# Kernel optimization log

Measured on AMD Instinct MI355X. Metric: run time of the kernel, lower is better.

## Reference

```python
import jax, jax.numpy as jnp
import numpy as np

EPS = 1e-5
NUM_HEADS = 12
PATCH = 16

def layernorm(x, g, b):
    m = jnp.mean(x, axis=-1, keepdims=True)
    v = jnp.var(x, axis=-1, keepdims=True)
    return (x - m) / jnp.sqrt(v + EPS) * g + b

def setup_inputs() -> dict:
    key = jax.random.key(0)
    ks = jax.random.split(key, 10)
    B, C, H, D, L = 32, 3, 224, 768, 12
    Dff, NCLS = 3072, 5
    N = (H // PATCH) ** 2 + 1  # 197 tokens incl. cls
    def rn(k, shape, s=0.02):
        return jax.random.normal(k, shape, jnp.float32) * s
    return {
        "x": jax.random.normal(ks[0], (B, C, H, H), jnp.float32),
        "conv_w": rn(ks[1], (D, C, PATCH, PATCH)),
        "conv_b": jnp.zeros((D,), jnp.float32),
        "cls_token": rn(ks[2], (1, 1, D)),
        "pos_embed": rn(ks[3], (1, N, D)),
        "ln1_g": jnp.ones((L, D), jnp.float32), "ln1_b": jnp.zeros((L, D), jnp.float32),
        "qkv_w": rn(ks[4], (L, D, 3 * D)), "qkv_b": jnp.zeros((L, 3 * D), jnp.float32),
        "proj_w": rn(ks[5], (L, D, D)), "proj_b": jnp.zeros((L, D), jnp.float32),
        "ln2_g": jnp.ones((L, D), jnp.float32), "ln2_b": jnp.zeros((L, D), jnp.float32),
        "fc1_w": rn(ks[6], (L, D, Dff)), "fc1_b": jnp.zeros((L, Dff), jnp.float32),
        "fc2_w": rn(ks[7], (L, Dff, D)), "fc2_b": jnp.zeros((L, D), jnp.float32),
        "norm_g": jnp.ones((D,), jnp.float32), "norm_b": jnp.zeros((D,), jnp.float32),
        "head_w": rn(ks[8], (D, NCLS)), "head_b": jnp.zeros((NCLS,), jnp.float32),
    }

def reference(x, conv_w, conv_b, cls_token, pos_embed,
              ln1_g, ln1_b, qkv_w, qkv_b, proj_w, proj_b,
              ln2_g, ln2_b, fc1_w, fc1_b, fc2_w, fc2_b,
              norm_g, norm_b, head_w, head_b):
    B = x.shape[0]
    D = conv_w.shape[0]
    HD = D // NUM_HEADS
    scale = HD ** -0.5
    # patch embedding: conv stride=kernel=16 -> [B, D, 14, 14]
    p = jax.lax.conv_general_dilated(
        x, conv_w, (PATCH, PATCH), 'VALID',
        dimension_numbers=('NCHW', 'OIHW', 'NCHW')) + conv_b[None, :, None, None]
    tok = p.reshape(B, D, -1).transpose(0, 2, 1)  # [B, Np, D]
    tok = jnp.concatenate([jnp.broadcast_to(cls_token, (B, 1, D)), tok], axis=1)
    tok = tok + pos_embed  # [B, N, D]; dropout is identity at eval

    def block(h, params):
        l1g, l1b, qw, qb, pw, pb, l2g, l2b, f1w, f1b, f2w, f2b = params
        y = layernorm(h, l1g, l1b)
        qkv = (y @ qw + qb).reshape(B, -1, 3, NUM_HEADS, HD)
        q, k, v = qkv[:, :, 0], qkv[:, :, 1], qkv[:, :, 2]  # [B, N, H, HD]
        attn = jax.nn.softmax(jnp.einsum('bqhd,bkhd->bhqk', q, k) * scale, axis=-1)
        o = jnp.einsum('bhqk,bkhd->bqhd', attn, v).reshape(B, -1, D)
        h = h + (o @ pw + pb)
        y = layernorm(h, l2g, l2b)
        h = h + (jax.nn.gelu(y @ f1w + f1b, approximate=False) @ f2w + f2b)
        return h, None

    tok, _ = jax.lax.scan(
        block, tok,
        (ln1_g, ln1_b, qkv_w, qkv_b, proj_w, proj_b,
         ln2_g, ln2_b, fc1_w, fc1_b, fc2_w, fc2_b))
    cls = layernorm(tok, norm_g, norm_b)[:, 0]  # [B, D]
    return cls @ head_w + head_b  # [B, num_classes]
```

## Files before the change

kernel.cpp:

```cpp
#include <hip/hip_runtime.h>
#include <hip/hip_bf16.h>
#include <math.h>

#define B_      32
#define NTOK    197
#define NPATCH  196
#define D_      768
#define DFF     3072
#define L_      12
#define NH      12
#define HD      64
#define NCLS    5
#define MTOK    (B_ * NTOK)
#define MPAD    6400
#define MPATCH  (B_ * NPATCH)
#define KPAD    224
#define KS_STR  72
#define VT_STR  232

typedef __attribute__((ext_vector_type(8))) short short8;
typedef __attribute__((ext_vector_type(4))) float floatx4;

static __device__ inline short f2bf(float f) {
  __hip_bfloat16 h = __float2bfloat16(f);
  short s; __builtin_memcpy(&s, &h, 2); return s;
}

__global__ __launch_bounds__(256) void cls_pos_kernel(
    const float* __restrict__ cls, const float* __restrict__ pos,
    float* __restrict__ tok) {
  int i = blockIdx.x * 256 + threadIdx.x;
  if (i < B_ * D_) {
    int b = i / D_, d = i % D_;
    tok[(size_t)b * NTOK * D_ + d] = cls[d] + pos[d];
  }
}

__global__ __launch_bounds__(256) void cvt_kernel(
    const float* __restrict__ src, short* __restrict__ dst, int n) {
  int i = blockIdx.x * 256 + threadIdx.x;
  if (i < n) dst[i] = f2bf(src[i]);
}

__global__ __launch_bounds__(256) void wconv_all_kernel(
    const float* __restrict__ qw, const float* __restrict__ pw,
    const float* __restrict__ f1w, const float* __restrict__ f2w,
    short* __restrict__ wq, short* __restrict__ wp,
    short* __restrict__ w1, short* __restrict__ w2) {
  int id = blockIdx.x;
  const float* W; short* Wt; int K, N, t;
  if (id < 1728)      { W = qw;  Wt = wq; K = 768;  N = 2304; t = id; }
  else if (id < 2304) { W = pw;  Wt = wp; K = 768;  N = 768;  t = id - 1728; }
  else if (id < 4608) { W = f1w; Wt = w1; K = 768;  N = 3072; t = id - 2304; }
  else                { W = f2w; Wt = w2; K = 3072; N = 768;  t = id - 4608; }
  int ntn = N >> 5;
  int k0 = (t / ntn) * 32, n0 = (t % ntn) * 32;
  __shared__ float tt[32][33];
  int tid = threadIdx.x;
#pragma unroll
  for (int q = 0; q < 4; q++) {
    int e = q * 256 + tid;
    int rk = e >> 5, cn = e & 31;
    tt[rk][cn] = W[(size_t)(k0 + rk) * N + n0 + cn];
  }
  __syncthreads();
#pragma unroll
  for (int q = 0; q < 4; q++) {
    int e = q * 256 + tid;
    int rn = e >> 5, ck = e & 31;
    Wt[(size_t)(n0 + rn) * K + k0 + ck] = f2bf(tt[ck][rn]);
  }
}

__global__ __launch_bounds__(256) void im2col_kernel(
    const float* __restrict__ x, short* __restrict__ Abf) {
  int i = blockIdx.x * 256 + threadIdx.x;
  if (i >= MPATCH * D_) return;
  int row = i / D_, col = i % D_;
  int b = row / NPATCH, n = row % NPATCH;
  int ph = n / 14, pw = n % 14;
  int c = col >> 8, r = col & 255;
  int kh = r >> 4, kw = r & 15;
  Abf[i] = f2bf(x[(((size_t)b * 3 + c) * 224 + (ph * 16 + kh)) * 224 + (pw * 16 + kw)]);
}

__global__ __launch_bounds__(256) void patch_scatter_kernel(
    const float* __restrict__ po, const float* __restrict__ pos,
    float* __restrict__ tok) {
  int i = blockIdx.x * 256 + threadIdx.x;
  if (i >= MPATCH * D_) return;
  int row = i / D_, col = i % D_;
  int b = row / NPATCH, n = row % NPATCH;
  tok[((size_t)b * NTOK + 1 + n) * D_ + col] = po[i] + pos[(size_t)(1 + n) * D_ + col];
}

template <bool OBF>
__global__ __launch_bounds__(256) void ln_kernel(
    const float* __restrict__ in, void* __restrict__ out,
    const float* __restrict__ g, const float* __restrict__ bt,
    long rs_in) {
  int row = blockIdx.x;
  const float* xr = in + (size_t)row * rs_in;
  int tid = threadIdx.x;
  float v0 = xr[tid], v1 = xr[tid + 256], v2 = xr[tid + 512];
  float s = v0 + v1 + v2;
#pragma unroll
  for (int off = 32; off; off >>= 1) s += __shfl_xor(s, off);
  __shared__ float red1[4], red2[4];
  int wid = tid >> 6, lane = tid & 63;
  if (lane == 0) red1[wid] = s;
  __syncthreads();
  float mean = (red1[0] + red1[1] + red1[2] + red1[3]) * (1.f / 768.f);
  float d0 = v0 - mean, d1 = v1 - mean, d2 = v2 - mean;
  float s2 = d0 * d0 + d1 * d1 + d2 * d2;
#pragma unroll
  for (int off = 32; off; off >>= 1) s2 += __shfl_xor(s2, off);
  if (lane == 0) red2[wid] = s2;
  __syncthreads();
  float var = (red2[0] + red2[1] + red2[2] + red2[3]) * (1.f / 768.f);
  float rstd = rsqrtf(var + 1e-5f);
  float o0 = d0 * rstd * g[tid]       + bt[tid];
  float o1 = d1 * rstd * g[tid + 256] + bt[tid + 256];
  float o2 = d2 * rstd * g[tid + 512] + bt[tid + 512];
  if (OBF) {
    short* yr = (short*)out + (size_t)row * D_;
    yr[tid] = f2bf(o0); yr[tid + 256] = f2bf(o1); yr[tid + 512] = f2bf(o2);
  } else {
    float* yr = (float*)out + (size_t)row * D_;
    yr[tid] = o0; yr[tid + 256] = o1; yr[tid + 512] = o2;
  }
}

template <int BM, bool OBF, bool RES, bool GELU_, bool SPLITK = false>
__global__ __launch_bounds__(256) void gemm_db_kernel(
    const short* __restrict__ A, const short* __restrict__ Wt,
    const float* __restrict__ bias, const float* __restrict__ res,
    void* __restrict__ Cout, int M, int N, int K, int kslice) {
  constexpr int NBI = (BM == 128) ? 2 : 4;
  __shared__ short As[2][BM * 32];
  __shared__ short Bs[2][128 * 32];
  const int tid = threadIdx.x;
  const int lane = tid & 63;
  const int wid = tid >> 6;
  const int wave_m = (BM == 128) ? (wid >> 1) : 0;
  const int wave_n = (BM == 128) ? (wid & 1) : wid;
  const int mbase = blockIdx.y * BM;
  const int nbase = blockIdx.x * 128;
  const int kbase = SPLITK ? blockIdx.z * kslice : 0;

  const int lrow = lane >> 2;
  const int kbg = (lane & 3) ^ ((lane >> 3) & 3);

  const short* gA0 = A + (size_t)(mbase + wid * 32 + lrow) * K + kbase + kbg * 8;
  const short* gA1 = gA0 + 16 * (size_t)K;
  const int brow0 = (BM == 128) ? (wid * 32) : (wid * 64);
  const short* gB[NBI];
  gB[0] = Wt + (size_t)(nbase + brow0 + lrow) * K + kbase + kbg * 8;
#pragma unroll
  for (int c = 1; c < NBI; c++) gB[c] = gB[0] + (size_t)c * 16 * K;

  typedef const __attribute__((address_space(1))) unsigned* gp_t;
  typedef __attribute__((address_space(3))) unsigned* lp_t;
  const int aoff = wid * 1024;
  const int boff = brow0 * 32;

  __builtin_amdgcn_global_load_lds((gp_t)(const void*)gA0, (lp_t)(void*)(&As[0][aoff]), 16, 0, 0);
  __builtin_amdgcn_global_load_lds((gp_t)(const void*)gA1, (lp_t)(void*)(&As[0][aoff + 512]), 16, 0, 0);
#pragma unroll
  for (int c = 0; c < NBI; c++)
    __builtin_amdgcn_global_load_lds((gp_t)(const void*)gB[c], (lp_t)(void*)(&Bs[0][boff + c * 512]), 16, 0, 0);

  floatx4 zero = {0.f, 0.f, 0.f, 0.f};
  floatx4 acc[4][4];
#pragma unroll
  for (int i = 0; i < 4; i++)
#pragma unroll
    for (int j = 0; j < 4; j++) acc[i][j] = zero;

  const int quad = lane >> 4;
  const int l15 = lane & 15;
  const int s = quad ^ ((l15 >> 1) & 3);

  const int niter = kslice >> 5;
  for (int it = 0; it < niter; it++) {
    const int cur = it & 1, nxt = cur ^ 1;
    __syncthreads();
    if (it + 1 < niter) {
      const int ks = (it + 1) << 5;
      __builtin_amdgcn_global_load_lds((gp_t)(const void*)(gA0 + ks), (lp_t)(void*)(&As[nxt][aoff]), 16, 0, 0);
      __builtin_amdgcn_global_load_lds((gp_t)(const void*)(gA1 + ks), (lp_t)(void*)(&As[nxt][aoff + 512]), 16, 0, 0);
#pragma unroll
      for (int c = 0; c < NBI; c++)
        __builtin_amdgcn_global_load_lds((gp_t)(const void*)(gB[c] + ks), (lp_t)(void*)(&Bs[nxt][boff + c * 512]), 16, 0, 0);
    }
    short8 a[4], b[4];
#pragma unroll
    for (int i = 0; i < 4; i++) {
      a[i] = *(const short8*)(&As[cur][(wave_m * 64 + i * 16 + l15) * 32 + s * 8]);
      b[i] = *(const short8*)(&Bs[cur][(wave_n * 64 + i * 16 + l15) * 32 + s * 8]);
    }
#pragma unroll
    for (int i = 0; i < 4; i++)
#pragma unroll
      for (int j = 0; j < 4; j++)
        acc[i][j] = __builtin_amdgcn_mfma_f32_16x16x32_bf16(a[i], b[j], acc[i][j], 0, 0, 0);
  }

#pragma unroll
  for (int i = 0; i < 4; i++) {
    int gm0 = mbase + wave_m * 64 + i * 16 + quad * 4;
#pragma unroll
    for (int r = 0; r < 4; r++) {
      int gm = gm0 + r;
      if (gm >= M) continue;
#pragma unroll
      for (int j = 0; j < 4; j++) {
        int gn = nbase + wave_n * 64 + j * 16 + l15;
        if constexpr (SPLITK) {
          ((float*)Cout)[(size_t)blockIdx.z * M * N + (size_t)gm * N + gn] = acc[i][j][r];
        } else {
          float c = acc[i][j][r] + bias[gn];
          if (RES) c += res[(size_t)gm * N + gn];
          if (GELU_) c = 0.5f * c * (1.f + erff(c * 0.70710678118654752f));
          if (OBF) ((short*)Cout)[(size_t)gm * N + gn] = f2bf(c);
          else ((float*)Cout)[(size_t)gm * N + gn] = c;
        }
      }
    }
  }
}

__global__ __launch_bounds__(256) void fc2_reduce_kernel(
    const float* __restrict__ part, const float* __restrict__ bias,
    float* __restrict__ tok) {
  const size_t MN = (size_t)MTOK * D_;
  size_t i = ((size_t)blockIdx.x * 256 + threadIdx.x) * 4;
  if (i >= MN) return;
  floatx4 p0 = *(const floatx4*)(part + i);
  floatx4 p1 = *(const floatx4*)(part + i + MN);
  floatx4 p2 = *(const floatx4*)(part + i + 2 * MN);
  floatx4 t  = *(const floatx4*)(tok + i);
  int col = (int)(i % D_);
  floatx4 o;
#pragma unroll
  for (int r = 0; r < 4; r++) o[r] = t[r] + bias[col + r] + p0[r] + p1[r] + p2[r];
  *(floatx4*)(tok + i) = o;
}

__global__ __launch_bounds__(256) void attn_mfma_kernel(
    const short* __restrict__ qkv, short* __restrict__ o) {
  __shared__ short Ks[KPAD * KS_STR];
  __shared__ short Vt[64 * VT_STR];
  __shared__ short Pw[4 * 16 * VT_STR];
  const int h = blockIdx.x % NH;
  const int b = blockIdx.x / NH;
  const int tid = threadIdx.x;
  const int lane = tid & 63, wid = tid >> 6;
  const size_t rowbase = (size_t)b * NTOK * (3 * D_);

  for (int it = 0; it < 7; it++) {
    int idx = it * 256 + tid;
    int dblk = idx / KPAD, key = idx % KPAD;
    int krow = key < NTOK ? key : NTOK - 1;
    const short* src = qkv + rowbase + (size_t)krow * (3 * D_) + h * HD;
    short8 kv = *(const short8*)(src + D_ + dblk * 8);
    *(short8*)(Ks + key * KS_STR + dblk * 8) = kv;
    short8 vv = *(const short8*)(src + 2 * D_ + dblk * 8);
#pragma unroll
    for (int i = 0; i < 8; i++) Vt[(dblk * 8 + i) * VT_STR + key] = vv[i];
  }
  __syncthreads();

  const int quad = lane >> 4, l15 = lane & 15;
  short* P = Pw + wid * 16 * VT_STR;
  const floatx4 zero = {0.f, 0.f, 0.f, 0.f};

  for (int qt = wid; qt < 14; qt += 4) {
    int qrow = qt * 16 + l15;
    int qr = qrow < NTOK ? qrow : NTOK - 1;
    const short* qbase = qkv + rowbase + (size_t)qr * (3 * D_) + h * HD;
    short8 a0 = *(const short8*)(qbase + quad * 8);
    short8 a1 = *(const short8*)(qbase + 32 + quad * 8);

    floatx4 s[14];
#pragma unroll
    for (int kt = 0; kt < 14; kt++) {
      const short* kb = Ks + (kt * 16 + l15) * KS_STR;
      short8 b0 = *(const short8*)(kb + quad * 8);
      short8 b1 = *(const short8*)(kb + 32 + quad * 8);
      floatx4 c = __builtin_amdgcn_mfma_f32_16x16x32_bf16(a0, b0, zero, 0, 0, 0);
      s[kt] = __builtin_amdgcn_mfma_f32_16x16x32_bf16(a1, b1, c, 0, 0, 0);
    }
#pragma unroll
    for (int kt = 0; kt < 14; kt++) {
      if (kt * 16 + l15 >= NTOK) {
#pragma unroll
        for (int r = 0; r < 4; r++) s[kt][r] = -1e30f;
      }
    }
    float mx[4] = {-1e30f, -1e30f, -1e30f, -1e30f};
#pragma unroll
    for (int kt = 0; kt < 14; kt++)
#pragma unroll
      for (int r = 0; r < 4; r++) mx[r] = fmaxf(mx[r], s[kt][r]);
#pragma unroll
    for (int off = 1; off < 16; off <<= 1)
#pragma unroll
      for (int r = 0; r < 4; r++) mx[r] = fmaxf(mx[r], __shfl_xor(mx[r], off));
    float lsum[4] = {0.f, 0.f, 0.f, 0.f};
#pragma unroll
    for (int kt = 0; kt < 14; kt++) {
#pragma unroll
      for (int r = 0; r < 4; r++) {
        float p = __expf(0.125f * (s[kt][r] - mx[r]));
        lsum[r] += p;
        P[(quad * 4 + r) * VT_STR + kt * 16 + l15] = f2bf(p);
      }
    }
#pragma unroll
    for (int off = 1; off < 16; off <<= 1)
#pragma unroll
      for (int r = 0; r < 4; r++) lsum[r] += __shfl_xor(lsum[r], off);
    float inv[4];
#pragma unroll
    for (int r = 0; r < 4; r++) inv[r] = 1.f / lsum[r];

    floatx4 oacc[4] = {zero, zero, zero, zero};
#pragma unroll
    for (int kk = 0; kk < 7; kk++) {
      short8 a = *(const short8*)(P + l15 * VT_STR + kk * 32 + quad * 8);
#pragma unroll
      for (int nt = 0; nt < 4; nt++) {
        short8 bv = *(const short8*)(Vt + (nt * 16 + l15) * VT_STR + kk * 32 + quad * 8);
        oacc[nt] = __builtin_amdgcn_mfma_f32_16x16x32_bf16(a, bv, oacc[nt], 0, 0, 0);
      }
    }
#pragma unroll
    for (int r = 0; r < 4; r++) {
      int q = qt * 16 + quad * 4 + r;
      if (q >= NTOK) continue;
      short* orow = o + ((size_t)(b * NTOK + q)) * D_ + h * HD;
#pragma unroll
      for (int nt = 0; nt < 4; nt++)
        orow[nt * 16 + l15] = f2bf(oacc[nt][r] * inv[r]);
    }
  }
}

__global__ __launch_bounds__(64) void head_kernel(
    const float* __restrict__ y, const float* __restrict__ hw,
    const float* __restrict__ hb, float* __restrict__ out) {
  int b = blockIdx.x;
  const float* yr = y + (size_t)b * D_;
  int lane = threadIdx.x;
  for (int j = 0; j < NCLS; j++) {
    float s = 0.f;
    for (int d = lane; d < D_; d += 64) s += yr[d] * hw[(size_t)d * NCLS + j];
#pragma unroll
    for (int off = 32; off; off >>= 1) s += __shfl_xor(s, off);
    if (lane == 0) out[b * NCLS + j] = s + hb[j];
  }
}

extern "C" void kernel_launch(void* const* d_in, const int* in_sizes, int n_in,
                              void* d_out, int out_size, void* d_ws, size_t ws_size,
                              hipStream_t stream) {
  const float* x        = (const float*)d_in[0];
  const float* conv_w   = (const float*)d_in[1];
  const float* conv_b   = (const float*)d_in[2];
  const float* cls_tok  = (const float*)d_in[3];
  const float* pos_emb  = (const float*)d_in[4];
  const float* ln1_g    = (const float*)d_in[5];
  const float* ln1_b    = (const float*)d_in[6];
  const float* qkv_w    = (const float*)d_in[7];
  const float* qkv_b    = (const float*)d_in[8];
  const float* proj_w   = (const float*)d_in[9];
  const float* proj_b   = (const float*)d_in[10];
  const float* ln2_g    = (const float*)d_in[11];
  const float* ln2_b    = (const float*)d_in[12];
  const float* fc1_w    = (const float*)d_in[13];
  const float* fc1_b    = (const float*)d_in[14];
  const float* fc2_w    = (const float*)d_in[15];
  const float* fc2_b    = (const float*)d_in[16];
  const float* norm_g   = (const float*)d_in[17];
  const float* norm_b   = (const float*)d_in[18];
  const float* head_w   = (const float*)d_in[19];
  const float* head_b   = (const float*)d_in[20];
  float* out = (float*)d_out;

  char* p = (char*)d_ws;
  float* tok    = (float*)p;                 p += (size_t)MTOK * D_ * 4;
  short* y_bf   = (short*)p;                 p += (size_t)MPAD * D_ * 2;
  short* o_bf   = (short*)p;                 p += (size_t)MPAD * D_ * 2;
  short* h_bf   = (short*)p;                 p += (size_t)MPAD * DFF * 2;
  short* wt_qkv = (short*)p;                 p += (size_t)D_ * 3 * D_ * 2;
  short* wt_prj = (short*)p;                 p += (size_t)D_ * D_ * 2;
  short* wt_fc1 = (short*)p;                 p += (size_t)D_ * DFF * 2;
  short* wt_fc2 = (short*)p;                 p += (size_t)DFF * D_ * 2;
  short* cw_bf  = (short*)p;                 p += (size_t)D_ * D_ * 2;
  short* im_bf  = (short*)p;                 p += (size_t)MPAD * D_ * 2;
  float* big1   = (float*)p;                 p += (size_t)MTOK * 3 * D_ * 4;
  short* qkv_bf = (short*)big1;
  float* pout   = big1;
  float* fc2_part = big1;
  float* yf     = (float*)(p);

  cvt_kernel<<<(D_ * D_ + 255) / 256, 256, 0, stream>>>(conv_w, cw_bf, D_ * D_);
  im2col_kernel<<<(MPATCH * D_ + 255) / 256, 256, 0, stream>>>(x, im_bf);
  cls_pos_kernel<<<(B_ * D_ + 255) / 256, 256, 0, stream>>>(cls_tok, pos_emb, tok);
  {
    dim3 g(D_ / 128, MPATCH / 64);
    gemm_db_kernel<64, false, false, false><<<g, 128, 0, stream>>>(
        im_bf, cw_bf, conv_b, nullptr, pout, MPATCH, D_, D_, D_);
  }
  patch_scatter_kernel<<<(MPATCH * D_ + 255) / 256, 256, 0, stream>>>(pout, pos_emb, tok);

  dim3 gQKV(3 * D_ / 128, (MTOK + 127) / 128);
  dim3 gPRJ(D_ / 128, (MTOK + 63) / 64);
  dim3 gFC1(DFF / 128, (MTOK + 127) / 128);
  dim3 gFC2(D_ / 128, (MTOK + 127) / 128, 3);

  for (int l = 0; l < L_; l++) {
    const float* l1g = ln1_g + l * D_;
    const float* l1b = ln1_b + l * D_;
    const float* qw  = qkv_w + (size_t)l * D_ * 3 * D_;
    const float* qb  = qkv_b + (size_t)l * 3 * D_;
    const float* pw  = proj_w + (size_t)l * D_ * D_;
    const float* pb  = proj_b + (size_t)l * D_;
    const float* l2g = ln2_g + l * D_;
    const float* l2b = ln2_b + l * D_;
    const float* f1w = fc1_w + (size_t)l * D_ * DFF;
    const float* f1b = fc1_b + (size_t)l * DFF;
    const float* f2w = fc2_w + (size_t)l * DFF * D_;
    const float* f2b = fc2_b + (size_t)l * D_;

    wconv_all_kernel<<<6912, 256, 0, stream>>>(qw, pw, f1w, f2w,
                                               wt_qkv, wt_prj, wt_fc1, wt_fc2);

    ln_kernel<true><<<MTOK, 256, 0, stream>>>(tok, y_bf, l1g, l1b, D_);
    gemm_db_kernel<128, true, false, false><<<gQKV, 256, 0, stream>>>(
        y_bf, wt_qkv, qb, nullptr, qkv_bf, MTOK, 3 * D_, D_, D_);
    attn_mfma_kernel<<<B_ * NH, 256, 0, stream>>>(qkv_bf, o_bf);
    gemm_db_kernel<64, false, true, false><<<gPRJ, 128, 0, stream>>>(
        o_bf, wt_prj, pb, tok, tok, MTOK, D_, D_, D_);
    ln_kernel<true><<<MTOK, 256, 0, stream>>>(tok, y_bf, l2g, l2b, D_);
    gemm_db_kernel<128, true, false, true><<<gFC1, 256, 0, stream>>>(
        y_bf, wt_fc1, f1b, nullptr, h_bf, MTOK, DFF, D_, D_);
    gemm_db_kernel<128, false, false, false, true><<<gFC2, 256, 0, stream>>>(
        h_bf, wt_fc2, nullptr, nullptr, fc2_part, MTOK, D_, DFF, 1024);
    fc2_reduce_kernel<<<(MTOK * D_ / 4 + 255) / 256, 256, 0, stream>>>(
        fc2_part, f2b, tok);
  }

  ln_kernel<false><<<B_, 256, 0, stream>>>(tok, yf, norm_g, norm_b, (long)NTOK * D_);
  head_kernel<<<B_, 64, 0, stream>>>(yf, head_w, head_b, out);
}
```

Measured before the change: 3.549 ms.

## Add 256x256-tile bf16 GEMM with direct global-to-LDS loads for QKV and FC1

Adds a new 512-thread GEMM kernel with 256x256 output tiles, 8 waves, and a double-buffered 128KB LDS pipeline. Loads go straight from global memory into LDS with global_load_lds, and the LDS layout is XOR-swizzled. Waits are managed by hand with s_waitcnt and barriers, and s_setprio raises priority around the MFMA bursts. QKV and FC1 now use this kernel in place of the 128-tile kernel, aiming for more operand reuse and less register-staging overhead. The trade-offs are fewer blocks (tile quantization: 25 row tiles over 6304 rows), much higher LDS use per block, and a reliance on fragile manual vmcnt counts. It also assumes the padded A buffer covers rows past M.

```diff
diff --git a/kernel.cpp b/kernel.cpp
--- a/kernel.cpp
+++ b/kernel.cpp
@@ -128,6 +128,141 @@
   } else {
     float* yr = (float*)out + (size_t)row * D_;
     yr[tid] = o0; yr[tid + 256] = o1; yr[tid + 512] = o2;
+  }
+}
+
+template <bool GELU_>
+__global__ __launch_bounds__(512, 2) void gemm256_kernel(
+    const short* __restrict__ A, const short* __restrict__ Wt,
+    const float* __restrict__ bias, short* __restrict__ Cout,
+    int M, int N, int K) {
+  __shared__ short lds[2 * 32768];
+  const int tid = threadIdx.x;
+  const int lane = tid & 63;
+  const int w = tid >> 6;
+  const int wave_m = w >> 2;
+  const int wave_n = w & 3;
+  const int mbase = blockIdx.y * 256;
+  const int nbase = blockIdx.x * 256;
+
+  const int lrow = lane >> 2;
+  const int kbg = (lane & 3) ^ ((lane >> 3) & 3);
+  const int quad = lane >> 4;
+  const int l15 = lane & 15;
+  const int s = quad ^ ((l15 >> 1) & 3);
+
+  const short* pAh[2];
+  pAh[0] = A + (size_t)(mbase + w * 16 + lrow) * K + kbg * 8;
+  pAh[1] = pAh[0] + (size_t)128 * K;
+  const short* pBh[2];
+  pBh[0] = Wt + (size_t)(nbase + w * 16 + lrow) * K + kbg * 8;
+  pBh[1] = pBh[0] + (size_t)128 * K;
+
+  typedef const __attribute__((address_space(1))) unsigned* gp_t;
+  typedef __attribute__((address_space(3))) unsigned* lp_t;
+
+#define STAGE(BUFOFF, Q, KOFF) do {                                          \
+    const int hi_ = (Q) & 1, ks_ = (Q) >> 1;                                 \
+    __builtin_amdgcn_global_load_lds(                                        \
+        (gp_t)(const void*)(pAh[hi_] + (KOFF) + ks_ * 32),                   \
+        (lp_t)(void*)(&lds[(BUFOFF) + ks_ * 8192 + (hi_ * 8 + w) * 512]),    \
+        16, 0, 0);                                                           \
+    __builtin_amdgcn_global_load_lds(                                        \
+        (gp_t)(const void*)(pBh[hi_] + (KOFF) + ks_ * 32),                   \
+        (lp_t)(void*)(&lds[(BUFOFF) + 16384 + ks_ * 8192 + (hi_ * 8 + w) * 512]), \
+        16, 0, 0);                                                           \
+  } while (0)
+
+  const int abase = (wave_m * 128 + l15) * 32 + s * 8;
+  const int bbase = 16384 + (wave_n * 64 + l15) * 32 + s * 8;
+
+#define LDA4(DST, CUROFF, KS, MF0)                                           \
+  _Pragma("unroll") for (int m_ = 0; m_ < 4; m_++)                           \
+      DST[m_] = *(const short8*)&lds[(CUROFF) + (KS) * 8192 + abase + ((MF0) + m_) * 512];
+#define LDB4(DST, CUROFF, KS)                                                \
+  _Pragma("unroll") for (int n_ = 0; n_ < 4; n_++)                           \
+      DST[n_] = *(const short8*)&lds[(CUROFF) + (KS) * 8192 + bbase + n_ * 512];
+#define MFMA16(MF0, AFR, BFR) do {                                           \
+    __builtin_amdgcn_s_setprio(1);                                           \
+    _Pragma("unroll") for (int m_ = 0; m_ < 4; m_++)                         \
+      _Pragma("unroll") for (int n_ = 0; n_ < 4; n_++)                       \
+        acc[(MF0) + m_][n_] = __builtin_amdgcn_mfma_f32_16x16x32_bf16(       \
+            AFR[m_], BFR[n_], acc[(MF0) + m_][n_], 0, 0, 0);                 \
+    __builtin_amdgcn_s_setprio(0);                                           \
+  } while (0)
+
+  floatx4 acc[8][4];
+#pragma unroll
+  for (int i = 0; i < 8; i++)
+#pragma unroll
+    for (int j = 0; j < 4; j++) acc[i][j] = floatx4{0.f, 0.f, 0.f, 0.f};
+
+  STAGE(0, 0, 0); STAGE(0, 1, 0); STAGE(0, 2, 0); STAGE(0, 3, 0);
+
+  const int NT = K >> 6;
+#pragma unroll 1
+  for (int kt = 0; kt < NT; kt++) {
+    const int cur = (kt & 1) * 32768;
+    const int nxtb = 32768 - cur;
+    const int koffn = (kt + 1) << 6;
+    const bool pref = (kt + 1 < NT);
+    short8 af[4], bf4[4];
+
+    if (pref) { STAGE(nxtb, 0, koffn); asm volatile("s_waitcnt vmcnt(6)" ::: "memory"); }
+    else      { asm volatile("s_waitcnt vmcnt(4)" ::: "memory"); }
+    __builtin_amdgcn_s_barrier();
+    asm volatile("" ::: "memory");
+    LDB4(bf4, cur, 0);
+    LDA4(af, cur, 0, 0);
+    MFMA16(0, af, bf4);
+    __builtin_amdgcn_s_barrier();
+
+    if (pref) STAGE(nxtb, 1, koffn);
+    LDA4(af, cur, 0, 4);
+    __builtin_amdgcn_s_barrier();
+    asm volatile("" ::: "memory");
+    MFMA16(4, af, bf4);
+    __builtin_amdgcn_s_barrier();
+
+    if (pref) { STAGE(nxtb, 2, koffn); asm volatile("s_waitcnt vmcnt(6)" ::: "memory"); }
+    else      { asm volatile("s_waitcnt vmcnt(0)" ::: "memory"); }
+    __builtin_amdgcn_s_barrier();
+    asm volatile("" ::: "memory");
+    LDB4(bf4, cur, 1);
+    LDA4(af, cur, 1, 0);
+    MFMA16(0, af, bf4);
+    __builtin_amdgcn_s_barrier();
+
+    if (pref) STAGE(nxtb, 3, koffn);
+    LDA4(af, cur, 1, 4);
+    __builtin_amdgcn_s_barrier();
+    asm volatile("" ::: "memory");
+    MFMA16(4, af, bf4);
+    __builtin_amdgcn_s_barrier();
+  }
+#undef STAGE
+#undef LDA4
+#undef LDB4
+#undef MFMA16
+
+  float bs[4];
+#pragma unroll
+  for (int nf = 0; nf < 4; nf++) bs[nf] = bias[nbase + wave_n * 64 + nf * 16 + l15];
+#pragma unroll
+  for (int mf = 0; mf < 8; mf++) {
+    int gm0 = mbase + wave_m * 128 + mf * 16 + quad * 4;
+#pragma unroll
+    for (int r = 0; r < 4; r++) {
+      int gm = gm0 + r;
+      if (gm >= M) continue;
+      short* crow = Cout + (size_t)gm * N + nbase + wave_n * 64;
+#pragma unroll
+      for (int nf = 0; nf < 4; nf++) {
+        float c = acc[mf][nf][r] + bs[nf];
+        if (GELU_) c = 0.5f * c * (1.f + erff(c * 0.70710678118654752f));
+        crow[nf * 16 + l15] = f2bf(c);
+      }
+    }
   }
 }
 
@@ -415,9 +550,9 @@
   }
   patch_scatter_kernel<<<(MPATCH * D_ + 255) / 256, 256, 0, stream>>>(pout, pos_emb, tok);
 
-  dim3 gQKV(3 * D_ / 128, (MTOK + 127) / 128);
+  dim3 gQKV(3 * D_ / 256, (MTOK + 255) / 256);
   dim3 gPRJ(D_ / 128, (MTOK + 63) / 64);
-  dim3 gFC1(DFF / 128, (MTOK + 127) / 128);
+  dim3 gFC1(DFF / 256, (MTOK + 255) / 256);
   dim3 gFC2(D_ / 128, (MTOK + 127) / 128, 3);
 
   for (int l = 0; l < L_; l++) {
@@ -438,14 +573,14 @@
                                                wt_qkv, wt_prj, wt_fc1, wt_fc2);
 
     ln_kernel<true><<<MTOK, 256, 0, stream>>>(tok, y_bf, l1g, l1b, D_);
-    gemm_db_kernel<128, true, false, false><<<gQKV, 256, 0, stream>>>(
-        y_bf, wt_qkv, qb, nullptr, qkv_bf, MTOK, 3 * D_, D_, D_);
+    gemm256_kernel<false><<<gQKV, 512, 0, stream>>>(
+        y_bf, wt_qkv, qb, qkv_bf, MTOK, 3 * D_, D_);
     attn_mfma_kernel<<<B_ * NH, 256, 0, stream>>>(qkv_bf, o_bf);
     gemm_db_kernel<64, false, true, false><<<gPRJ, 128, 0, stream>>>(
         o_bf, wt_prj, pb, tok, tok, MTOK, D_, D_, D_);
     ln_kernel<true><<<MTOK, 256, 0, stream>>>(tok, y_bf, l2g, l2b, D_);
-    gemm_db_kernel<128, true, false, true><<<gFC1, 256, 0, stream>>>(
-        y_bf, wt_fc1, f1b, nullptr, h_bf, MTOK, DFF, D_, D_);
+    gemm256_kernel<true><<<gFC1, 512, 0, stream>>>(
+        y_bf, wt_fc1, f1b, h_bf, MTOK, DFF, D_);
     gemm_db_kernel<128, false, false, false, true><<<gFC2, 256, 0, stream>>>(
         h_bf, wt_fc2, nullptr, nullptr, fc2_part, MTOK, D_, DFF, 1024);
     fc2_reduce_kernel<<<(MTOK * D_ / 4 + 255) / 256, 256, 0, stream>>>(
```

Measured after the change: 3.545 ms. No clear change (-0.1%).

## Triple-buffer GEMM LDS pipeline and fuse split-K reduce with next-layer LayerNorm

Applied to the files above, without the earlier changes.

The GEMM main loop moves from double to triple buffering of LDS tiles. It waits on explicit vmcnt counts instead of a full __syncthreads, so loads run two stages ahead, and it raises wave priority around the MFMA block. Separately, the FC2 split-K reduction is fused with the next layer's LN1, which removes one LayerNorm launch and one read of the token tensor per layer. The extra LDS stage raises shared memory use, which may lower occupancy. The hand-set vmcnt values depend on how many loads each stage issues.

```diff
diff --git a/kernel.cpp b/kernel.cpp
--- a/kernel.cpp
+++ b/kernel.cpp
@@ -137,8 +137,8 @@
     const float* __restrict__ bias, const float* __restrict__ res,
     void* __restrict__ Cout, int M, int N, int K, int kslice) {
   constexpr int NBI = (BM == 128) ? 2 : 4;
-  __shared__ short As[2][BM * 32];
-  __shared__ short Bs[2][128 * 32];
+  __shared__ short As[3][BM * 32];
+  __shared__ short Bs[3][128 * 32];
   const int tid = threadIdx.x;
   const int lane = tid & 63;
   const int wid = tid >> 6;
@@ -164,11 +164,19 @@
   const int aoff = wid * 1024;
   const int boff = brow0 * 32;
 
-  __builtin_amdgcn_global_load_lds((gp_t)(const void*)gA0, (lp_t)(void*)(&As[0][aoff]), 16, 0, 0);
-  __builtin_amdgcn_global_load_lds((gp_t)(const void*)gA1, (lp_t)(void*)(&As[0][aoff + 512]), 16, 0, 0);
-#pragma unroll
-  for (int c = 0; c < NBI; c++)
-    __builtin_amdgcn_global_load_lds((gp_t)(const void*)gB[c], (lp_t)(void*)(&Bs[0][boff + c * 512]), 16, 0, 0);
+#define STG(BUF, KS) do {                                                      \
+    __builtin_amdgcn_global_load_lds((gp_t)(const void*)(gA0 + (KS)),          \
+        (lp_t)(void*)(&As[BUF][aoff]), 16, 0, 0);                              \
+    __builtin_amdgcn_global_load_lds((gp_t)(const void*)(gA1 + (KS)),          \
+        (lp_t)(void*)(&As[BUF][aoff + 512]), 16, 0, 0);                        \
+    _Pragma("unroll") for (int c = 0; c < NBI; c++)                            \
+      __builtin_amdgcn_global_load_lds((gp_t)(const void*)(gB[c] + (KS)),      \
+          (lp_t)(void*)(&Bs[BUF][boff + c * 512]), 16, 0, 0);                  \
+  } while (0)
+
+  const int niter = kslice >> 5;
+  STG(0, 0);
+  if (niter > 1) STG(1, 32);
 
   floatx4 zero = {0.f, 0.f, 0.f, 0.f};
   floatx4 acc[4][4];
@@ -181,30 +189,35 @@
   const int l15 = lane & 15;
   const int s = quad ^ ((l15 >> 1) & 3);
 
-  const int niter = kslice >> 5;
+  int cur = 0, nxt2 = 2;
+#pragma unroll 1
   for (int it = 0; it < niter; it++) {
-    const int cur = it & 1, nxt = cur ^ 1;
-    __syncthreads();
     if (it + 1 < niter) {
-      const int ks = (it + 1) << 5;
-      __builtin_amdgcn_global_load_lds((gp_t)(const void*)(gA0 + ks), (lp_t)(void*)(&As[nxt][aoff]), 16, 0, 0);
-      __builtin_amdgcn_global_load_lds((gp_t)(const void*)(gA1 + ks), (lp_t)(void*)(&As[nxt][aoff + 512]), 16, 0, 0);
-#pragma unroll
-      for (int c = 0; c < NBI; c++)
-        __builtin_amdgcn_global_load_lds((gp_t)(const void*)(gB[c] + ks), (lp_t)(void*)(&Bs[nxt][boff + c * 512]), 16, 0, 0);
-    }
+      if constexpr (BM == 128) asm volatile("s_waitcnt vmcnt(4)" ::: "memory");
+      else                     asm volatile("s_waitcnt vmcnt(6)" ::: "memory");
+    } else {
+      asm volatile("s_waitcnt vmcnt(0)" ::: "memory");
+    }
+    __builtin_amdgcn_s_barrier();
+    asm volatile("" ::: "memory");
+    if (it + 2 < niter) STG(nxt2, (it + 2) << 5);
     short8 a[4], b[4];
 #pragma unroll
     for (int i = 0; i < 4; i++) {
       a[i] = *(const short8*)(&As[cur][(wave_m * 64 + i * 16 + l15) * 32 + s * 8]);
       b[i] = *(const short8*)(&Bs[cur][(wave_n * 64 + i * 16 + l15) * 32 + s * 8]);
     }
+    __builtin_amdgcn_s_setprio(1);
 #pragma unroll
     for (int i = 0; i < 4; i++)
 #pragma unroll
       for (int j = 0; j < 4; j++)
         acc[i][j] = __builtin_amdgcn_mfma_f32_16x16x32_bf16(a[i], b[j], acc[i][j], 0, 0, 0);
-  }
+    __builtin_amdgcn_s_setprio(0);
+    cur = (cur == 2) ? 0 : cur + 1;
+    nxt2 = (nxt2 == 2) ? 0 : nxt2 + 1;
+  }
+#undef STG
 
 #pragma unroll
   for (int i = 0; i < 4; i++) {
@@ -230,21 +243,44 @@
   }
 }
 
-__global__ __launch_bounds__(256) void fc2_reduce_kernel(
-    const float* __restrict__ part, const float* __restrict__ bias,
-    float* __restrict__ tok) {
+template <bool LNOUT>
+__global__ __launch_bounds__(256) void fc2ln_kernel(
+    const float* __restrict__ part, const float* __restrict__ fbias,
+    float* __restrict__ tok, const float* __restrict__ g,
+    const float* __restrict__ bt, short* __restrict__ yout) {
   const size_t MN = (size_t)MTOK * D_;
-  size_t i = ((size_t)blockIdx.x * 256 + threadIdx.x) * 4;
-  if (i >= MN) return;
-  floatx4 p0 = *(const floatx4*)(part + i);
-  floatx4 p1 = *(const floatx4*)(part + i + MN);
-  floatx4 p2 = *(const floatx4*)(part + i + 2 * MN);
-  floatx4 t  = *(const floatx4*)(tok + i);
-  int col = (int)(i % D_);
-  floatx4 o;
-#pragma unroll
-  for (int r = 0; r < 4; r++) o[r] = t[r] + bias[col + r] + p0[r] + p1[r] + p2[r];
-  *(floatx4*)(tok + i) = o;
+  int row = blockIdx.x;
+  int tid = threadIdx.x;
+  size_t base = (size_t)row * D_;
+  float t0, t1, t2;
+  {
+    size_t i0 = base + tid, i1 = base + tid + 256, i2 = base + tid + 512;
+    t0 = tok[i0] + fbias[tid]       + part[i0] + part[i0 + MN] + part[i0 + 2 * MN];
+    t1 = tok[i1] + fbias[tid + 256] + part[i1] + part[i1 + MN] + part[i1 + 2 * MN];
+    t2 = tok[i2] + fbias[tid + 512] + part[i2] + part[i2 + MN] + part[i2 + 2 * MN];
+    tok[i0] = t0; tok[i1] = t1; tok[i2] = t2;
+  }
+  if constexpr (!LNOUT) return;
+  float s = t0 + t1 + t2;
+#pragma unroll
+  for (int off = 32; off; off >>= 1) s += __shfl_xor(s, off);
+  __shared__ float red1[4], red2[4];
+  int wid = tid >> 6, lane = tid & 63;
+  if (lane == 0) red1[wid] = s;
+  __syncthreads();
+  float mean = (red1[0] + red1[1] + red1[2] + red1[3]) * (1.f / 768.f);
+  float d0 = t0 - mean, d1 = t1 - mean, d2 = t2 - mean;
+  float s2 = d0 * d0 + d1 * d1 + d2 * d2;
+#pragma unroll
+  for (int off = 32; off; off >>= 1) s2 += __shfl_xor(s2, off);
+  if (lane == 0) red2[wid] = s2;
+  __syncthreads();
+  float var = (red2[0] + red2[1] + red2[2] + red2[3]) * (1.f / 768.f);
+  float rstd = rsqrtf(var + 1e-5f);
+  short* yr = yout + (size_t)row * D_;
+  yr[tid]       = f2bf(d0 * rstd * g[tid]       + bt[tid]);
+  yr[tid + 256] = f2bf(d1 * rstd * g[tid + 256] + bt[tid + 256]);
+  yr[tid + 512] = f2bf(d2 * rstd * g[tid + 512] + bt[tid + 512]);
 }
 
 __global__ __launch_bounds__(256) void attn_mfma_kernel(
@@ -437,7 +473,8 @@
     wconv_all_kernel<<<6912, 256, 0, stream>>>(qw, pw, f1w, f2w,
                                                wt_qkv, wt_prj, wt_fc1, wt_fc2);
 
-    ln_kernel<true><<<MTOK, 256, 0, stream>>>(tok, y_bf, l1g, l1b, D_);
+    if (l == 0)
+      ln_kernel<true><<<MTOK, 256, 0, stream>>>(tok, y_bf, l1g, l1b, D_);
     gemm_db_kernel<128, true, false, false><<<gQKV, 256, 0, stream>>>(
         y_bf, wt_qkv, qb, nullptr, qkv_bf, MTOK, 3 * D_, D_, D_);
     attn_mfma_kernel<<<B_ * NH, 256, 0, stream>>>(qkv_bf, o_bf);
@@ -448,8 +485,12 @@
         y_bf, wt_fc1, f1b, nullptr, h_bf, MTOK, DFF, D_, D_);
     gemm_db_kernel<128, false, false, false, true><<<gFC2, 256, 0, stream>>>(
         h_bf, wt_fc2, nullptr, nullptr, fc2_part, MTOK, D_, DFF, 1024);
-    fc2_reduce_kernel<<<(MTOK * D_ / 4 + 255) / 256, 256, 0, stream>>>(
-        fc2_part, f2b, tok);
+    if (l + 1 < L_)
+      fc2ln_kernel<true><<<MTOK, 256, 0, stream>>>(
+          fc2_part, f2b, tok, ln1_g + (l + 1) * D_, ln1_b + (l + 1) * D_, y_bf);
+    else
+      fc2ln_kernel<false><<<MTOK, 256, 0, stream>>>(
+          fc2_part, f2b, tok, nullptr, nullptr, nullptr);
   }
 
   ln_kernel<false><<<B_, 256, 0, stream>>>(tok, yf, norm_g, norm_b, (long)NTOK * D_);
```

After: 3.549 ms. About the same (+0.0%).
